# Performance work log

Measured on AMD Instinct MI355X. Metric: run time of the kernel, lower is better.

The kernel has to match this reference:

```python
import jax, jax.numpy as jnp
import numpy as np

N_NODES = 2000
GCN_OUT = 8
HID = 256
N_STEPS_OUT = 4


def setup_inputs() -> dict:
    key = jax.random.key(0)
    ks = jax.random.split(key, 16)
    B, S, N, E, F, H = 32, 24, N_NODES, 16000, GCN_OUT, HID
    I = F * N  # LSTM input size = gcn_out_features * num_nodes
    s = 0.05
    inp = {
        "x_sequences": jax.random.normal(ks[0], (B, S, N), jnp.float32),
        "edge_index": jax.random.randint(ks[1], (B, S, 2, E), 0, N, jnp.int32),
        "edge_distances": jax.random.uniform(ks[2], (B, S, E), jnp.float32),
        # CustomGCNLayer params (linear 1->F)
        "W_gcn": jax.random.normal(ks[3], (1, F), jnp.float32) * s,
        "b_gcn": jnp.zeros((F,), jnp.float32),
        # 2-layer LSTM (PyTorch layout: [4H, in], gate order i,f,g,o)
        "Wih0": jax.random.normal(ks[4], (4 * H, I), jnp.float32) * s,
        "Whh0": jax.random.normal(ks[5], (4 * H, H), jnp.float32) * s,
        "bih0": jnp.zeros((4 * H,), jnp.float32),
        "bhh0": jnp.zeros((4 * H,), jnp.float32),
        "Wih1": jax.random.normal(ks[6], (4 * H, H), jnp.float32) * s,
        "Whh1": jax.random.normal(ks[7], (4 * H, H), jnp.float32) * s,
        "bih1": jnp.zeros((4 * H,), jnp.float32),
        "bhh1": jnp.zeros((4 * H,), jnp.float32),
        # fc: hidden -> n_steps_out * num_nodes * num_node_features
        "fc_W": jax.random.normal(ks[8], (N_STEPS_OUT * N, H), jnp.float32) * s,
        "fc_b": jnp.zeros((N_STEPS_OUT * N,), jnp.float32),
    }
    return inp


def _lstm_layer(x, Wih, Whh, bih, bhh):
    # x: [B, S, in] -> hs: [B, S, H]
    B = x.shape[0]
    H = Whh.shape[1]
    b = bih + bhh

    def step(carry, xt):
        h, c = carry
        gates = xt @ Wih.T + h @ Whh.T + b  # [B, 4H]
        i, f, g, o = jnp.split(gates, 4, axis=-1)
        i = jax.nn.sigmoid(i)
        f = jax.nn.sigmoid(f)
        g = jnp.tanh(g)
        o = jax.nn.sigmoid(o)
        c = f * c + i * g
        h = o * jnp.tanh(c)
        return (h, c), h

    init = (jnp.zeros((B, H), x.dtype), jnp.zeros((B, H), x.dtype))
    _, hs = jax.lax.scan(step, init, x.transpose(1, 0, 2))  # time-major
    return hs.transpose(1, 0, 2)


def reference(x_sequences, edge_index, edge_distances, W_gcn, b_gcn,
              Wih0, Whh0, bih0, bhh0, Wih1, Whh1, bih1, bhh1, fc_W, fc_b):
    B, S, N = x_sequences.shape
    F = W_gcn.shape[1]
    # GCN layer (batched over all B*S graph snapshots):
    # h = x @ W + b ; out[i] = sum_{(j->i)} dist_e * h[j]
    h = x_sequences[..., None] * W_gcn[0] + b_gcn        # [B,S,N,F]
    src = edge_index[:, :, 0].reshape(B * S, -1)         # [BS,E]
    dst = edge_index[:, :, 1].reshape(B * S, -1)
    dist = edge_distances.reshape(B * S, -1)
    h2 = h.reshape(B * S, N, F)
    msgs = jnp.take_along_axis(h2, src[:, :, None], axis=1) * dist[..., None]  # [BS,E,F]
    agg = jax.vmap(lambda m, d: jax.ops.segment_sum(m, d, num_segments=N))(msgs, dst)
    gcn_seq = jnp.tanh(agg.reshape(B, S, N * F))         # [B,S,N*F]

    h1 = _lstm_layer(gcn_seq, Wih0, Whh0, bih0, bhh0)
    h2l = _lstm_layer(h1, Wih1, Whh1, bih1, bhh1)
    last = jnp.tanh(h2l)[:, -1, :]                       # [B,H]
    out = last @ fc_W.T + fc_b                           # [B, n_steps_out*N]
    n_steps_out = fc_b.shape[0] // N
    return out.reshape(B, n_steps_out, N)                # num_node_features=1 squeezed
```

## Files before the change

### kernel.cpp

```cpp
#include <hip/hip_runtime.h>

#define DEVINL __device__ __forceinline__

typedef __attribute__((ext_vector_type(8))) short bf16x8;
typedef __attribute__((ext_vector_type(4))) float f32x4;
typedef _Float16 half2_t __attribute__((ext_vector_type(2)));
typedef _Float16 f16x8 __attribute__((ext_vector_type(8)));

DEVINL unsigned short f2bf(float f) {
  unsigned int u = __float_as_uint(f);
  u += 0x7FFFu + ((u >> 16) & 1u);
  return (unsigned short)(u >> 16);
}
DEVINL unsigned short f2h(float f) {
  return __builtin_bit_cast(unsigned short, (_Float16)f);
}
DEVINL float sigmf(float x) { return 1.f / (1.f + __expf(-x)); }
DEVINL float tanh_fast(float x) { float e = __expf(2.f * x); return 1.f - 2.f / (e + 1.f); }

DEVINL float fdot2u(unsigned int h, unsigned int w, float acc) {
  return __builtin_amdgcn_fdot2(__builtin_bit_cast(half2_t, h),
                                __builtin_bit_cast(half2_t, w), acc, false);
}

DEVINL void gload_lds16(const void* g, void* l) {
  __builtin_amdgcn_global_load_lds(
      (const __attribute__((address_space(1))) void*)g,
      (__attribute__((address_space(3))) void*)l, 16, 0, 0);
}

#define FXSCALE 1048576.f
#define FXINV   (1.f / 1048576.f)

__global__ __launch_bounds__(1024) void fused_pre(
    const float* __restrict__ x, const int* __restrict__ ei, const float* __restrict__ ed,
    const float* __restrict__ Wg, const float* __restrict__ bg,
    unsigned short* __restrict__ G,
    const float* __restrict__ Wih0, unsigned short* __restrict__ W0bf,
    const float* __restrict__ Whh0, uint2* __restrict__ WPG0,
    const float* __restrict__ Whh1, uint2* __restrict__ WPG1,
    const float* __restrict__ Wih1, unsigned short* __restrict__ W1h) {
  __shared__ float xs[2000];
  __shared__ int Ai[2000];
  __shared__ int Di[2000];
  int blk = blockIdx.x;
  int tid = threadIdx.x;

  if (blk < 768) {
    int bs = blk;
    for (int i = tid; i < 2000; i += 1024) {
      xs[i] = x[(size_t)bs * 2000 + i];
      Ai[i] = 0; Di[i] = 0;
    }
    bool bgz = (bg[0] == 0.f) && (bg[1] == 0.f) && (bg[2] == 0.f) && (bg[3] == 0.f) &&
               (bg[4] == 0.f) && (bg[5] == 0.f) && (bg[6] == 0.f) && (bg[7] == 0.f);
    __syncthreads();
    const int4* srcp = (const int4*)(ei + (size_t)bs * 32000);
    const int4* dstp = (const int4*)(ei + (size_t)bs * 32000 + 16000);
    const float4* dp = (const float4*)(ed + (size_t)bs * 16000);
    if (bgz) {
      for (int i = tid; i < 4000; i += 1024) {
        int4 s4 = srcp[i];
        int4 d4 = dstp[i];
        float4 w4 = dp[i];
        atomicAdd(&Ai[d4.x], __float2int_rn(w4.x * xs[s4.x] * FXSCALE));
        atomicAdd(&Ai[d4.y], __float2int_rn(w4.y * xs[s4.y] * FXSCALE));
        atomicAdd(&Ai[d4.z], __float2int_rn(w4.z * xs[s4.z] * FXSCALE));
        atomicAdd(&Ai[d4.w], __float2int_rn(w4.w * xs[s4.w] * FXSCALE));
      }
    } else {
      for (int i = tid; i < 4000; i += 1024) {
        int4 s4 = srcp[i];
        int4 d4 = dstp[i];
        float4 w4 = dp[i];
        atomicAdd(&Ai[d4.x], __float2int_rn(w4.x * xs[s4.x] * FXSCALE));
        atomicAdd(&Di[d4.x], __float2int_rn(w4.x * FXSCALE));
        atomicAdd(&Ai[d4.y], __float2int_rn(w4.y * xs[s4.y] * FXSCALE));
        atomicAdd(&Di[d4.y], __float2int_rn(w4.y * FXSCALE));
        atomicAdd(&Ai[d4.z], __float2int_rn(w4.z * xs[s4.z] * FXSCALE));
        atomicAdd(&Di[d4.z], __float2int_rn(w4.z * FXSCALE));
        atomicAdd(&Ai[d4.w], __float2int_rn(w4.w * xs[s4.w] * FXSCALE));
        atomicAdd(&Di[d4.w], __float2int_rn(w4.w * FXSCALE));
      }
    }
    __syncthreads();
    float wreg[8], breg[8];
#pragma unroll
    for (int f = 0; f < 8; ++f) { wreg[f] = Wg[f]; breg[f] = bg[f]; }
    for (int n = tid; n < 2000; n += 1024) {
      float a  = (float)Ai[n] * FXINV;
      float dd = (float)Di[n] * FXINV;
      unsigned int u[4];
#pragma unroll
      for (int p = 0; p < 4; ++p) {
        float v0 = tanh_fast(wreg[2 * p] * a + breg[2 * p] * dd);
        float v1 = tanh_fast(wreg[2 * p + 1] * a + breg[2 * p + 1] * dd);
        u[p] = (unsigned int)f2bf(v0) | ((unsigned int)f2bf(v1) << 16);
      }
      *(uint4*)&G[(size_t)bs * 16000 + n * 8] = make_uint4(u[0], u[1], u[2], u[3]);
    }
  } else if (blk < 1768) {
    int base = (blk - 768) * 1024 + tid;
#pragma unroll
    for (int k = 0; k < 4; ++k) {
      int id = base + k * 1024000;
      float4 v = *(const float4*)&Wih0[(size_t)id * 4];
      unsigned int a = (unsigned int)f2bf(v.x) | ((unsigned int)f2bf(v.y) << 16);
      unsigned int b = (unsigned int)f2bf(v.z) | ((unsigned int)f2bf(v.w) << 16);
      *(uint2*)&W0bf[(size_t)id * 4] = make_uint2(a, b);
    }
  } else if (blk < 1896) {
    const float* in = (blk < 1832) ? Whh0 : Whh1;
    uint2* outp = (blk < 1832) ? WPG0 : WPG1;
    int id = ((blk < 1832) ? (blk - 1768) : (blk - 1832)) * 1024 + tid;
    int g = id >> 14;
    int rem = id & 16383;
    int u2 = rem >> 8;
    int c = rem & 255;
    int col = (c >> 6) * 256 + g * 64 + (c & 63);
    float4 v = *(const float4*)&in[col * 256 + u2 * 4];
    unsigned int p0 = (unsigned int)f2h(v.x) | ((unsigned int)f2h(v.y) << 16);
    unsigned int p1 = (unsigned int)f2h(v.z) | ((unsigned int)f2h(v.w) << 16);
    outp[id] = make_uint2(p0, p1);
  } else {
    int id = (blk - 1896) * 1024 + tid;
    W1h[id] = f2h(Wih1[id]);
  }
}

__global__ __launch_bounds__(256) void gemm_bt(
    const unsigned short* __restrict__ A, const unsigned short* __restrict__ B,
    float* __restrict__ Cp) {
  __shared__ __align__(16) unsigned short As[2][128 * 32];
  __shared__ __align__(16) unsigned short Bs[2][128 * 32];
  const int K = 16000;
  int nt = blockIdx.x;
  int mt = blockIdx.y;
  int ks = blockIdx.z;
  int m0 = mt * 128, n0 = nt * 128;
  int tid = threadIdx.x;
  int lane = tid & 63;
  int w = tid >> 6;
  int wm = (w >> 1) * 64, wn = (w & 1) * 64;
  int fr = lane & 15;
  int kg = lane >> 4;

  f32x4 acc[4][4] = {};
  const unsigned short* Ag = A + (size_t)m0 * K + ks * 1600;
  const unsigned short* Bg = B + (size_t)n0 * K + ks * 1600;

  int row0 = tid >> 2,            ko0 = (tid & 3) * 8,        cb0 = (tid & ~63);
  int row1 = (256 + tid) >> 2,    ko1 = (tid & 3) * 8,        cb1 = 256 + (tid & ~63);

#define STAGE_BT(buf, kk)                                                     \
  do {                                                                        \
    gload_lds16(&Ag[(size_t)row0 * K + (kk) + ko0], &As[buf][cb0 * 8]);       \
    gload_lds16(&Bg[(size_t)row0 * K + (kk) + ko0], &Bs[buf][cb0 * 8]);       \
    gload_lds16(&Ag[(size_t)row1 * K + (kk) + ko1], &As[buf][cb1 * 8]);       \
    gload_lds16(&Bg[(size_t)row1 * K + (kk) + ko1], &Bs[buf][cb1 * 8]);       \
  } while (0)

  STAGE_BT(0, 0);
#pragma unroll 1
  for (int it = 0; it < 50; ++it) {
    int cur = it & 1;
    if (it < 49) {
      STAGE_BT(cur ^ 1, (it + 1) * 32);
      asm volatile("s_waitcnt vmcnt(4)" ::: "memory");
    } else {
      asm volatile("s_waitcnt vmcnt(0)" ::: "memory");
    }
    __builtin_amdgcn_s_barrier();
    __builtin_amdgcn_sched_barrier(0);
    bf16x8 aF[4], bF[4];
#pragma unroll
    for (int i = 0; i < 4; ++i)
      aF[i] = *(const bf16x8*)&As[cur][(wm + i * 16 + fr) * 32 + kg * 8];
#pragma unroll
    for (int i = 0; i < 4; ++i)
      bF[i] = *(const bf16x8*)&Bs[cur][(wn + i * 16 + fr) * 32 + kg * 8];
#pragma unroll
    for (int i = 0; i < 4; ++i)
#pragma unroll
      for (int j = 0; j < 4; ++j)
        acc[i][j] = __builtin_amdgcn_mfma_f32_16x16x32_bf16(aF[i], bF[j], acc[i][j], 0, 0, 0);
    __builtin_amdgcn_s_barrier();
  }
#undef STAGE_BT
  float* Co = Cp + (size_t)ks * 768 * 1024;
  int mr = (lane >> 4) * 4;
#pragma unroll
  for (int i = 0; i < 4; ++i)
#pragma unroll
    for (int j = 0; j < 4; ++j) {
      int n = n0 + wn + j * 16 + fr;
#pragma unroll
      for (int r = 0; r < 4; ++r) {
        int m = m0 + wm + i * 16 + mr + r;
        Co[(size_t)m * 1024 + n] = acc[i][j][r];
      }
    }
}

__global__ __launch_bounds__(256) void reduce_z0(
    const float* __restrict__ Cp, const float* __restrict__ bih,
    const float* __restrict__ bhh, float* __restrict__ Z0) {
  int id = blockIdx.x * 256 + threadIdx.x;
  float s = bih[id & 1023] + bhh[id & 1023];
#pragma unroll
  for (int p = 0; p < 10; ++p) s += Cp[(size_t)p * 786432 + id];
  Z0[id] = s;
}

__global__ __launch_bounds__(1024) void lstm_sync2(
    const float* __restrict__ Z, const uint2* __restrict__ WPG,
    unsigned int* __restrict__ Hex, unsigned short* __restrict__ Hout,
    float* __restrict__ lastOut, int tagBase) {
  __shared__ __align__(16) uint2 Wl2[64 * 256];
  __shared__ float gparts[1024];
  __shared__ __align__(8) unsigned short h16[256];
  int bid = blockIdx.x;
  int b = bid & 31, g = bid >> 5;
  int tid = threadIdx.x;
  int lane = tid & 63;
  int c = tid & 255;
  int kh = __builtin_amdgcn_readfirstlane(tid >> 8);
  int q = c >> 6, r = c & 63;
  int col = q * 256 + g * 64 + r;

  const uint2* wsrc = WPG + (size_t)g * 16384;
  for (int i = tid; i < 16384; i += 1024) Wl2[i] = wsrc[i];
  if (tid < 128) ((unsigned int*)h16)[tid] = 0;
  __syncthreads();

  float cst = 0.f;
  const size_t b24 = (size_t)b * 24;

#pragma unroll 1
  for (int t = 0; t < 24; ++t) {
    uint2 hv = *(const uint2*)&((const unsigned int*)h16)[lane * 2];
    float acc = (kh == 0) ? Z[(b24 + t) * 1024 + col] : 0.f;
#pragma unroll
    for (int j = 0; j < 16; ++j) {
      const int u2i = kh * 16 + j;
      uint2 w2 = Wl2[u2i * 256 + c];
      unsigned int h0 = (unsigned int)__builtin_amdgcn_readlane((int)hv.x, u2i);
      unsigned int h1 = (unsigned int)__builtin_amdgcn_readlane((int)hv.y, u2i);
      acc = fdot2u(h0, w2.x, acc);
      acc = fdot2u(h1, w2.y, acc);
    }
    gparts[tid] = acc;
    __syncthreads();
    unsigned int* HexS = Hex + (t & 1) * 8192 + b * 256;
    if (tid < 64) {
      float i_ = gparts[tid]       + gparts[tid + 256]  + gparts[tid + 512]  + gparts[tid + 768];
      float f_ = gparts[tid + 64]  + gparts[tid + 320]  + gparts[tid + 576]  + gparts[tid + 832];
      float g_ = gparts[tid + 128] + gparts[tid + 384]  + gparts[tid + 640]  + gparts[tid + 896];
      float o_ = gparts[tid + 192] + gparts[tid + 448]  + gparts[tid + 704]  + gparts[tid + 960];
      float ig = sigmf(i_), fg = sigmf(f_);
      float gg = tanh_fast(g_), og = sigmf(o_);
      cst = fg * cst + ig * gg;
      float h = og * tanh_fast(cst);
      unsigned short hh = f2h(h);
      h16[g * 64 + tid] = hh;
      __hip_atomic_store(&HexS[g * 64 + tid],
                         (unsigned int)hh | ((unsigned int)(tagBase + t + 1) << 16),
                         __ATOMIC_RELAXED, __HIP_MEMORY_SCOPE_AGENT);
      if (Hout) Hout[(b24 + t) * 256 + g * 64 + tid] = hh;
      if (lastOut && t == 23) lastOut[b * 256 + g * 64 + tid] = tanh_fast(h);
    }
    if (t == 23) break;
    if (tid < 256 && (tid >> 6) != g) {
      const unsigned int tag = (unsigned int)(tagBase + t + 1);
      unsigned int v;
      do {
        v = __hip_atomic_load(&HexS[tid], __ATOMIC_RELAXED, __HIP_MEMORY_SCOPE_AGENT);
      } while ((v >> 16) != tag);
      h16[tid] = (unsigned short)(v & 0xFFFFu);
    }
    __syncthreads();
  }
}

__global__ __launch_bounds__(256) void gemm_z1_mfma(
    const unsigned short* __restrict__ A, const unsigned short* __restrict__ B,
    const float* __restrict__ bih, const float* __restrict__ bhh,
    float* __restrict__ Z1) {
  __shared__ __align__(16) unsigned short As[128 * 32];
  __shared__ __align__(16) unsigned short Bs[128 * 32];
  const int K = 256;
  int nt = blockIdx.x;
  int mt = blockIdx.y;
  int m0 = mt * 128, n0 = nt * 128;
  int tid = threadIdx.x;
  int lane = tid & 63;
  int w = tid >> 6;
  int wm = (w >> 1) * 64, wn = (w & 1) * 64;
  int fr = lane & 15;
  int kg = lane >> 4;

  f32x4 acc[4][4] = {};
  const unsigned short* Ag = A + (size_t)m0 * K;
  const unsigned short* Bg = B + (size_t)n0 * K;

  for (int kk = 0; kk < 256; kk += 32) {
#pragma unroll
    for (int q = 0; q < 2; ++q) {
      int c = q * 256 + tid;
      int row = c >> 2;
      int ko = (c & 3) * 8;
      int cb = q * 256 + (tid & ~63);
      gload_lds16(&Ag[(size_t)row * K + kk + ko], &As[cb * 8]);
      gload_lds16(&Bg[(size_t)row * K + kk + ko], &Bs[cb * 8]);
    }
    __syncthreads();
    f16x8 aF[4], bF[4];
#pragma unroll
    for (int i = 0; i < 4; ++i)
      aF[i] = *(const f16x8*)&As[(wm + i * 16 + fr) * 32 + kg * 8];
#pragma unroll
    for (int i = 0; i < 4; ++i)
      bF[i] = *(const f16x8*)&Bs[(wn + i * 16 + fr) * 32 + kg * 8];
#pragma unroll
    for (int i = 0; i < 4; ++i)
#pragma unroll
      for (int j = 0; j < 4; ++j)
        acc[i][j] = __builtin_amdgcn_mfma_f32_16x16x32_f16(aF[i], bF[j], acc[i][j], 0, 0, 0);
    __syncthreads();
  }
  int mr = (lane >> 4) * 4;
#pragma unroll
  for (int j = 0; j < 4; ++j) {
    int n = n0 + wn + j * 16 + fr;
    float bias = bih[n] + bhh[n];
#pragma unroll
    for (int i = 0; i < 4; ++i) {
#pragma unroll
      for (int r = 0; r < 4; ++r) {
        int m = m0 + wm + i * 16 + mr + r;
        Z1[(size_t)m * 1024 + n] = acc[i][j][r] + bias;
      }
    }
  }
}

__global__ __launch_bounds__(256) void fc_kernel(
    const float* __restrict__ last, const float* __restrict__ fcW,
    const float* __restrict__ fcb, float* __restrict__ out) {
  __shared__ float ls[8][256];
  int tid = threadIdx.x;
  int o = blockIdx.x * 256 + tid;
  int b0 = blockIdx.y * 8;
  for (int i = tid; i < 2048; i += 256)
    ls[i >> 8][i & 255] = last[(b0 + (i >> 8)) * 256 + (i & 255)];
  __syncthreads();
  if (o < 8000) {
    float acc[8] = {};
    for (int k = 0; k < 256; k += 4) {
      float4 wv = *(const float4*)&fcW[(size_t)o * 256 + k];
#pragma unroll
      for (int b = 0; b < 8; ++b)
        acc[b] += wv.x * ls[b][k] + wv.y * ls[b][k + 1] + wv.z * ls[b][k + 2] + wv.w * ls[b][k + 3];
    }
    float bias = fcb[o];
#pragma unroll
    for (int b = 0; b < 8; ++b) out[(size_t)(b0 + b) * 8000 + o] = acc[b] + bias;
  }
}

extern "C" void kernel_launch(void* const* d_in, const int* in_sizes, int n_in,
                              void* d_out, int out_size, void* d_ws, size_t ws_size,
                              hipStream_t stream) {
  const float* x    = (const float*)d_in[0];
  const int*   ei   = (const int*)d_in[1];
  const float* ed   = (const float*)d_in[2];
  const float* Wg   = (const float*)d_in[3];
  const float* bg   = (const float*)d_in[4];
  const float* Wih0 = (const float*)d_in[5];
  const float* Whh0 = (const float*)d_in[6];
  const float* bih0 = (const float*)d_in[7];
  const float* bhh0 = (const float*)d_in[8];
  const float* Wih1 = (const float*)d_in[9];
  const float* Whh1 = (const float*)d_in[10];
  const float* bih1 = (const float*)d_in[11];
  const float* bhh1 = (const float*)d_in[12];
  const float* fcW  = (const float*)d_in[13];
  const float* fcb  = (const float*)d_in[14];
  float* out = (float*)d_out;

  char* ws = (char*)d_ws;
  unsigned short* Gbf  = (unsigned short*)(ws);
  unsigned short* W0bf = (unsigned short*)(ws + 24576000);
  float* Zpart = (float*)(ws + 57344000);
  float* Z0    = (float*)(ws + 88801280);
  uint2* WPG0  = (uint2*)(ws + 91947008);
  uint2* WPG1  = (uint2*)(ws + 92471296);
  unsigned short* W1h = (unsigned short*)(ws + 92995584);
  unsigned short* H1  = (unsigned short*)(ws + 94044160);
  float* Z1    = (float*)(ws + 94830592);
  float* lastb = (float*)(ws + 97976320);
  unsigned int* Hex0 = (unsigned int*)(ws + 98009088);
  unsigned int* Hex1 = (unsigned int*)(ws + 98074624);

  hipMemsetAsync(Hex0, 0, 131072, stream);
  fused_pre<<<2152, 1024, 0, stream>>>(x, ei, ed, Wg, bg, Gbf,
                                       Wih0, W0bf, Whh0, WPG0, Whh1, WPG1,
                                       Wih1, (unsigned short*)W1h);
  gemm_bt<<<dim3(8, 6, 10), 256, 0, stream>>>(Gbf, W0bf, Zpart);
  reduce_z0<<<3072, 256, 0, stream>>>(Zpart, bih0, bhh0, Z0);
  lstm_sync2<<<128, 1024, 0, stream>>>(Z0, WPG0, Hex0, H1, nullptr, 0);
  gemm_z1_mfma<<<dim3(8, 6), 256, 0, stream>>>(H1, W1h, bih1, bhh1, Z1);
  lstm_sync2<<<128, 1024, 0, stream>>>(Z1, WPG1, Hex1, nullptr, lastb, 100);
  fc_kernel<<<dim3(32, 4), 256, 0, stream>>>(lastb, fcW, fcb, out);
}
```

Baseline: 232.6 us.

## Fuse split-K partial reduction into LSTM layer-0 kernel and interleave pre-kernel blocks

Removes the separate reduce_z0 kernel. The first LSTM recurrence kernel now sums the 10 split-K partials plus the biases directly from Zpart at each timestep, which saves one launch and one round trip through global memory. In exchange, ten loads now sit on the serial recurrence path each step, although they are issued before the dot product so the latency can overlap. Separately, fused_pre now interleaves GCN blocks with Wih0 conversion blocks, so the block dispatcher mixes atomic-heavy and bandwidth-heavy work.

```diff
diff --git a/kernel.cpp b/kernel.cpp
--- a/kernel.cpp
+++ b/kernel.cpp
@@ -46,8 +46,8 @@
   int blk = blockIdx.x;
   int tid = threadIdx.x;
 
-  if (blk < 768) {
-    int bs = blk;
+  if (blk < 1536 && (blk & 1) == 0) {
+    int bs = blk >> 1;
     for (int i = tid; i < 2000; i += 1024) {
       xs[i] = x[(size_t)bs * 2000 + i];
       Ai[i] = 0; Di[i] = 0;
@@ -100,7 +100,8 @@
       *(uint4*)&G[(size_t)bs * 16000 + n * 8] = make_uint4(u[0], u[1], u[2], u[3]);
     }
   } else if (blk < 1768) {
-    int base = (blk - 768) * 1024 + tid;
+    int j = (blk < 1536) ? (blk >> 1) : (768 + (blk - 1536));
+    int base = j * 1024 + tid;
 #pragma unroll
     for (int k = 0; k < 4; ++k) {
       int id = base + k * 1024000;
@@ -202,18 +203,10 @@
     }
 }
 
-__global__ __launch_bounds__(256) void reduce_z0(
-    const float* __restrict__ Cp, const float* __restrict__ bih,
-    const float* __restrict__ bhh, float* __restrict__ Z0) {
-  int id = blockIdx.x * 256 + threadIdx.x;
-  float s = bih[id & 1023] + bhh[id & 1023];
-#pragma unroll
-  for (int p = 0; p < 10; ++p) s += Cp[(size_t)p * 786432 + id];
-  Z0[id] = s;
-}
-
 __global__ __launch_bounds__(1024) void lstm_sync2(
-    const float* __restrict__ Z, const uint2* __restrict__ WPG,
+    const float* __restrict__ Z, const float* __restrict__ Cp,
+    const float* __restrict__ bih, const float* __restrict__ bhh,
+    const uint2* __restrict__ WPG,
     unsigned int* __restrict__ Hex, unsigned short* __restrict__ Hout,
     float* __restrict__ lastOut, int tagBase) {
   __shared__ __align__(16) uint2 Wl2[64 * 256];
@@ -231,6 +224,7 @@
   const uint2* wsrc = WPG + (size_t)g * 16384;
   for (int i = tid; i < 16384; i += 1024) Wl2[i] = wsrc[i];
   if (tid < 128) ((unsigned int*)h16)[tid] = 0;
+  float biasc = (Cp != nullptr && kh == 0) ? (bih[col] + bhh[col]) : 0.f;
   __syncthreads();
 
   float cst = 0.f;
@@ -239,7 +233,19 @@
 #pragma unroll 1
   for (int t = 0; t < 24; ++t) {
     uint2 hv = *(const uint2*)&((const unsigned int*)h16)[lane * 2];
-    float acc = (kh == 0) ? Z[(b24 + t) * 1024 + col] : 0.f;
+    float z = 0.f;
+    if (kh == 0) {
+      if (Cp != nullptr) {
+        size_t off = (b24 + t) * 1024 + col;
+        float s = biasc;
+#pragma unroll
+        for (int p = 0; p < 10; ++p) s += Cp[(size_t)p * 786432 + off];
+        z = s;
+      } else {
+        z = Z[(b24 + t) * 1024 + col];
+      }
+    }
+    float acc = 0.f;
 #pragma unroll
     for (int j = 0; j < 16; ++j) {
       const int u2i = kh * 16 + j;
@@ -249,7 +255,7 @@
       acc = fdot2u(h0, w2.x, acc);
       acc = fdot2u(h1, w2.y, acc);
     }
-    gparts[tid] = acc;
+    gparts[tid] = acc + z;
     __syncthreads();
     unsigned int* HexS = Hex + (t & 1) * 8192 + b * 256;
     if (tid < 64) {
@@ -392,7 +398,6 @@
   unsigned short* Gbf  = (unsigned short*)(ws);
   unsigned short* W0bf = (unsigned short*)(ws + 24576000);
   float* Zpart = (float*)(ws + 57344000);
-  float* Z0    = (float*)(ws + 88801280);
   uint2* WPG0  = (uint2*)(ws + 91947008);
   uint2* WPG1  = (uint2*)(ws + 92471296);
   unsigned short* W1h = (unsigned short*)(ws + 92995584);
@@ -407,9 +412,10 @@
                                        Wih0, W0bf, Whh0, WPG0, Whh1, WPG1,
                                        Wih1, (unsigned short*)W1h);
   gemm_bt<<<dim3(8, 6, 10), 256, 0, stream>>>(Gbf, W0bf, Zpart);
-  reduce_z0<<<3072, 256, 0, stream>>>(Zpart, bih0, bhh0, Z0);
-  lstm_sync2<<<128, 1024, 0, stream>>>(Z0, WPG0, Hex0, H1, nullptr, 0);
+  lstm_sync2<<<128, 1024, 0, stream>>>(nullptr, Zpart, bih0, bhh0, WPG0,
+                                       Hex0, H1, nullptr, 0);
   gemm_z1_mfma<<<dim3(8, 6), 256, 0, stream>>>(H1, W1h, bih1, bhh1, Z1);
-  lstm_sync2<<<128, 1024, 0, stream>>>(Z1, WPG1, Hex1, nullptr, lastb, 100);
+  lstm_sync2<<<128, 1024, 0, stream>>>(Z1, nullptr, nullptr, nullptr, WPG1,
+                                       Hex1, nullptr, lastb, 100);
   fc_kernel<<<dim3(32, 4), 256, 0, stream>>>(lastb, fcW, fcb, out);
 }
```

Result: no change. 236.8 us (+1.8%).
